# Kernel optimization log

Hardware: AMD Instinct MI355X
Metric: run time of the kernel (lower is better)

## Reference

```python
import jax, jax.numpy as jnp
import numpy as np

N_NODES = 50000
N_EDGES = 800000
HIDDEN = 256          # hidden_size == output_size (same `inputs` feeds all projections)
NUM_HEADS = 8
D_K = HIDDEN // NUM_HEADS  # 32
SCALE = float(np.sqrt(D_K))


def setup_inputs() -> dict:
    key = jax.random.key(0)
    ks = jax.random.split(key, 8)
    w_std = 1.0 / np.sqrt(HIDDEN)
    inputs = jax.random.normal(ks[0], (N_NODES, HIDDEN), jnp.float32)
    src = jax.random.randint(ks[1], (N_EDGES,), 0, N_NODES, dtype=jnp.int32)
    # guarantee every node has >= 1 in-edge (avoid 0/0 in normalization)
    dst_rand = jax.random.randint(ks[2], (N_EDGES - N_NODES,), 0, N_NODES, dtype=jnp.int32)
    dst = jnp.concatenate([jnp.arange(N_NODES, dtype=jnp.int32), dst_rand])
    Wq = jax.random.normal(ks[3], (HIDDEN, HIDDEN), jnp.float32) * w_std
    bq = jnp.zeros((HIDDEN,), jnp.float32)
    Wk = jax.random.normal(ks[4], (HIDDEN, HIDDEN), jnp.float32) * w_std
    Wv = jax.random.normal(ks[5], (HIDDEN, HIDDEN), jnp.float32) * w_std
    Wo = jax.random.normal(ks[6], (HIDDEN, HIDDEN), jnp.float32) * w_std
    bo = jnp.zeros((HIDDEN,), jnp.float32)
    return {"inputs": inputs, "Wq": Wq, "bq": bq, "Wk": Wk, "Wv": Wv,
            "Wo": Wo, "bo": bo, "src": src, "dst": dst}


def reference(inputs, Wq, bq, Wk, Wv, Wo, bo, src, dst):
    n = inputs.shape[0]
    # projections (dropout is identity in eval mode)
    q = (inputs @ Wq.T + bq).reshape(n, NUM_HEADS, D_K)
    k = (inputs @ Wk.T).reshape(n, NUM_HEADS, D_K)
    v = (inputs @ Wv.T).reshape(n, NUM_HEADS, D_K)
    # edge-wise dot product score: k[src] . q[dst]  -> [E, H]
    score = jnp.einsum('ehd,ehd->eh', k[src], q[dst])
    score = jnp.exp(jnp.clip(score / SCALE, -10.0, 10.0))
    # weighted segment-sum aggregation over in-edges of each dst node
    wv = jax.ops.segment_sum(v[src] * score[..., None], dst, num_segments=n)  # [N,H,dk]
    z = jax.ops.segment_sum(score, dst, num_segments=n)                        # [N,H]
    o = (wv / z[..., None]).reshape(n, HIDDEN)
    return o @ Wo.T + bo
```

## Files before the change

kernel.cpp:

```cpp
#include <hip/hip_runtime.h>
#include <hip/hip_bf16.h>
#include <math.h>

#define HIDDEN 256
#define INV_SCALE 0.17677669529663687f

typedef __attribute__((ext_vector_type(8))) short short8;
typedef __attribute__((ext_vector_type(4))) float f32x4;
typedef const __attribute__((address_space(1))) unsigned int* gas_ptr;
typedef __attribute__((address_space(3))) unsigned int* las_ptr;

static __device__ __forceinline__ unsigned short f2bf(float x) {
  unsigned u = __float_as_uint(x);
  unsigned r = (u + 0x7FFF + ((u >> 16) & 1)) >> 16;
  return (unsigned short)r;
}
static __device__ __forceinline__ float bf2f(unsigned short u) {
  return __uint_as_float((unsigned)u << 16);
}


__global__ __launch_bounds__(256) void conv_a_kernel(const float* __restrict__ in,
                                                     unsigned short* __restrict__ out,
                                                     int total4) {
  int stride = gridDim.x * blockDim.x;
  for (int i = blockIdx.x * blockDim.x + threadIdx.x; i < total4; i += stride) {
    float4 f = ((const float4*)in)[i];
    ushort4 u;
    u.x = f2bf(f.x); u.y = f2bf(f.y); u.z = f2bf(f.z); u.w = f2bf(f.w);
    ((ushort4*)out)[i] = u;
  }
}

__global__ __launch_bounds__(256) void conv_w_kernel(const float* __restrict__ Wq,
                                                     const float* __restrict__ Wk,
                                                     const float* __restrict__ Wv,
                                                     const float* __restrict__ Wo,
                                                     unsigned short* __restrict__ wqkv,
                                                     unsigned short* __restrict__ wob) {
  int i = blockIdx.x * 256 + threadIdx.x;
  int m = i >> 16;
  int j = i & 65535;
  const float* s = (m == 0) ? Wq : (m == 1) ? Wk : (m == 2) ? Wv : Wo;
  unsigned short b = f2bf(s[j]);
  if (m < 3) wqkv[m * 65536 + j] = b;
  else wob[j] = b;
}


__global__ __launch_bounds__(256) void hist_kernel(const int* __restrict__ dst,
                                                   int* __restrict__ deg, int E) {
  int e = blockIdx.x * blockDim.x + threadIdx.x;
  if (e < E) atomicAdd(&deg[dst[e]], 1);
}

__global__ __launch_bounds__(256) void scan1_kernel(const int* __restrict__ deg,
                                                    int* __restrict__ offs,
                                                    int* __restrict__ bsums, int N) {
  __shared__ int s[256];
  int tid = threadIdx.x;
  int base = blockIdx.x * 1024 + tid * 4;
  int v0 = (base + 0 < N) ? deg[base + 0] : 0;
  int v1 = (base + 1 < N) ? deg[base + 1] : 0;
  int v2 = (base + 2 < N) ? deg[base + 2] : 0;
  int v3 = (base + 3 < N) ? deg[base + 3] : 0;
  int tsum = v0 + v1 + v2 + v3;
  s[tid] = tsum;
  __syncthreads();
  for (int off = 1; off < 256; off <<= 1) {
    int t = (tid >= off) ? s[tid - off] : 0;
    __syncthreads();
    s[tid] += t;
    __syncthreads();
  }
  int excl = s[tid] - tsum;
  if (base + 0 < N) offs[base + 0] = excl;
  if (base + 1 < N) offs[base + 1] = excl + v0;
  if (base + 2 < N) offs[base + 2] = excl + v0 + v1;
  if (base + 3 < N) offs[base + 3] = excl + v0 + v1 + v2;
  if (tid == 255) bsums[blockIdx.x] = s[255];
}

__global__ void scan2_kernel(int* __restrict__ bsums, int nb) {
  if (blockIdx.x == 0 && threadIdx.x == 0) {
    int run = 0;
    for (int b = 0; b < nb; ++b) { int t = bsums[b]; bsums[b] = run; run += t; }
  }
}

__global__ __launch_bounds__(256) void scan3_kernel(int* __restrict__ offs,
                                                    int* __restrict__ cursor,
                                                    const int* __restrict__ bsums,
                                                    int N, int E) {
  int i = blockIdx.x * blockDim.x + threadIdx.x;
  if (i < N) {
    int v = offs[i] + bsums[i >> 10];
    offs[i] = v;
    cursor[i] = v;
  }
  if (i == 0) offs[N] = E;
}

__global__ __launch_bounds__(256) void scatter_kernel(const int* __restrict__ dst,
                                                      const int* __restrict__ src,
                                                      int* __restrict__ cursor,
                                                      int* __restrict__ esrc, int E) {
  int e = blockIdx.x * blockDim.x + threadIdx.x;
  if (e < E) {
    int n = dst[e];
    int pos = atomicAdd(&cursor[n], 1);
    esrc[pos] = src[e];
  }
}

#define GBM 128
#define GBN 128
#define GBK 32
#define NKSTEP (HIDDEN / GBK)

template <int MODE>
__global__ __launch_bounds__(256) void mfma_gemm_kernel(const unsigned short* __restrict__ A,
                                                        const unsigned short* __restrict__ B,
                                                        const float* __restrict__ bias,
                                                        float* __restrict__ Cf,
                                                        unsigned short* __restrict__ Cq,
                                                        unsigned short* __restrict__ Ck,
                                                        unsigned short* __restrict__ Cv,
                                                        int M) {
  __shared__ unsigned short As[2][GBM][GBK];
  __shared__ unsigned short Bs[2][GBN][GBK];
  int tid = threadIdx.x;
  int lane = tid & 63;
  int wid = tid >> 6;
  int wm = wid >> 1, wn = wid & 1;
  int brow = blockIdx.x * GBM;
  int bcol = blockIdx.y * GBN;

  int srow = wid * 32 + (lane >> 2);
  int skoff = (lane & 3) * 8;
  const unsigned short* gA0 = &A[(size_t)(brow + srow) * HIDDEN + skoff];
  const unsigned short* gB0 = &B[(size_t)(bcol + srow) * HIDDEN + skoff];
  char* ldsA0 = (char*)&As[0][0][0] + wid * 2048;
  char* ldsA1 = (char*)&As[1][0][0] + wid * 2048;
  char* ldsB0 = (char*)&Bs[0][0][0] + wid * 2048;
  char* ldsB1 = (char*)&Bs[1][0][0] + wid * 2048;

  f32x4 acc[4][4] = {};

  int fr = lane & 15;
  int kg = (lane >> 4) * 8;

  {
    const unsigned short* a = gA0;
    const unsigned short* b = gB0;
    __builtin_amdgcn_global_load_lds((gas_ptr)(const void*)a, (las_ptr)(void*)ldsA0, 16, 0, 0);
    __builtin_amdgcn_global_load_lds((gas_ptr)(const void*)(a + 16 * HIDDEN), (las_ptr)(void*)(ldsA0 + 1024), 16, 0, 0);
    __builtin_amdgcn_global_load_lds((gas_ptr)(const void*)b, (las_ptr)(void*)ldsB0, 16, 0, 0);
    __builtin_amdgcn_global_load_lds((gas_ptr)(const void*)(b + 16 * HIDDEN), (las_ptr)(void*)(ldsB0 + 1024), 16, 0, 0);
  }

#pragma unroll
  for (int t = 0; t < NKSTEP; ++t) {
    int p = t & 1;
    if (t + 1 < NKSTEP) {
      int k1 = (t + 1) * GBK;
      const unsigned short* a = gA0 + k1;
      const unsigned short* b = gB0 + k1;
      char* dA = p ? ldsA0 : ldsA1;
      char* dB = p ? ldsB0 : ldsB1;
      __builtin_amdgcn_global_load_lds((gas_ptr)(const void*)a, (las_ptr)(void*)dA, 16, 0, 0);
      __builtin_amdgcn_global_load_lds((gas_ptr)(const void*)(a + 16 * HIDDEN), (las_ptr)(void*)(dA + 1024), 16, 0, 0);
      __builtin_amdgcn_global_load_lds((gas_ptr)(const void*)b, (las_ptr)(void*)dB, 16, 0, 0);
      __builtin_amdgcn_global_load_lds((gas_ptr)(const void*)(b + 16 * HIDDEN), (las_ptr)(void*)(dB + 1024), 16, 0, 0);
      asm volatile("s_waitcnt vmcnt(4)" ::: "memory");
    } else {
      asm volatile("s_waitcnt vmcnt(0)" ::: "memory");
    }
    __builtin_amdgcn_s_barrier();
    __builtin_amdgcn_sched_barrier(0);
    short8 af[4], bfg[4];
#pragma unroll
    for (int mi = 0; mi < 4; ++mi)
      af[mi] = *(const short8*)&As[p][wm * 64 + mi * 16 + fr][kg];
#pragma unroll
    for (int ni = 0; ni < 4; ++ni)
      bfg[ni] = *(const short8*)&Bs[p][wn * 64 + ni * 16 + fr][kg];
#pragma unroll
    for (int mi = 0; mi < 4; ++mi)
#pragma unroll
      for (int ni = 0; ni < 4; ++ni)
        acc[mi][ni] = __builtin_amdgcn_mfma_f32_16x16x32_bf16(af[mi], bfg[ni], acc[mi][ni], 0, 0, 0);
    __builtin_amdgcn_s_barrier();
  }

  int fq = lane >> 4;
#pragma unroll
  for (int mi = 0; mi < 4; ++mi) {
#pragma unroll
    for (int ni = 0; ni < 4; ++ni) {
      int c = bcol + wn * 64 + ni * 16 + fr;
#pragma unroll
      for (int j = 0; j < 4; ++j) {
        int r = brow + wm * 64 + mi * 16 + fq * 4 + j;
        if (r < M) {
          float val = acc[mi][ni][j];
          if (MODE == 1) {
            Cf[(size_t)r * HIDDEN + c] = val + bias[c];
          } else {
            if (c < 256) Cq[(size_t)r * HIDDEN + c] = f2bf(val + bias[c]);
            else if (c < 512) Ck[(size_t)r * HIDDEN + (c - 256)] = f2bf(val);
            else Cv[(size_t)r * HIDDEN + (c - 512)] = f2bf(val);
          }
        }
      }
    }
  }
}

__global__ __launch_bounds__(256) void agg_kernel(const unsigned short* __restrict__ q,
                                                  const unsigned short* __restrict__ k,
                                                  const unsigned short* __restrict__ v,
                                                  const int* __restrict__ offs,
                                                  const int* __restrict__ esrc,
                                                  unsigned short* __restrict__ o, int N) {
  int n = blockIdx.x * 4 + (threadIdx.x >> 6);
  if (n >= N) return;
  int lane = threadIdx.x & 63;
  int half = lane >> 5;
  int l = lane & 31;

  float qf[8];
  {
    ushort4 qa = *(const ushort4*)&q[(size_t)n * HIDDEN + l * 8];
    ushort4 qb = *(const ushort4*)&q[(size_t)n * HIDDEN + l * 8 + 4];
    qf[0] = bf2f(qa.x); qf[1] = bf2f(qa.y); qf[2] = bf2f(qa.z); qf[3] = bf2f(qa.w);
    qf[4] = bf2f(qb.x); qf[5] = bf2f(qb.y); qf[6] = bf2f(qb.z); qf[7] = bf2f(qb.w);
  }

  int e0 = offs[n], e1 = offs[n + 1];
  float wv[8] = {};
  float z = 0.f;

  for (int idx = e0; idx < e1; idx += 2) {
    int my = idx + half;
    bool valid = my < e1;
    int s = esrc[valid ? my : idx];
    const ushort4* kp = (const ushort4*)&k[(size_t)s * HIDDEN + l * 8];
    const ushort4* vp = (const ushort4*)&v[(size_t)s * HIDDEN + l * 8];
    ushort4 ka = kp[0], kb = kp[1];
    ushort4 va = vp[0], vb = vp[1];
    float dot = qf[0] * bf2f(ka.x) + qf[1] * bf2f(ka.y) + qf[2] * bf2f(ka.z) + qf[3] * bf2f(ka.w)
              + qf[4] * bf2f(kb.x) + qf[5] * bf2f(kb.y) + qf[6] * bf2f(kb.z) + qf[7] * bf2f(kb.w);
    dot += __shfl_xor(dot, 1);
    dot += __shfl_xor(dot, 2);
    float e = 0.f;
    if (valid) e = __expf(fminf(fmaxf(dot * INV_SCALE, -10.f), 10.f));
    wv[0] += e * bf2f(va.x); wv[1] += e * bf2f(va.y);
    wv[2] += e * bf2f(va.z); wv[3] += e * bf2f(va.w);
    wv[4] += e * bf2f(vb.x); wv[5] += e * bf2f(vb.y);
    wv[6] += e * bf2f(vb.z); wv[7] += e * bf2f(vb.w);
    z += e;
  }

#pragma unroll
  for (int j = 0; j < 8; ++j) wv[j] += __shfl_xor(wv[j], 32);
  z += __shfl_xor(z, 32);

  if (half == 0) {
    float inv = 1.0f / z;
    ushort4 o0, o1;
    o0.x = f2bf(wv[0] * inv); o0.y = f2bf(wv[1] * inv);
    o0.z = f2bf(wv[2] * inv); o0.w = f2bf(wv[3] * inv);
    o1.x = f2bf(wv[4] * inv); o1.y = f2bf(wv[5] * inv);
    o1.z = f2bf(wv[6] * inv); o1.w = f2bf(wv[7] * inv);
    ushort4* op = (ushort4*)&o[(size_t)n * HIDDEN + l * 8];
    op[0] = o0; op[1] = o1;
  }
}


extern "C" void kernel_launch(void* const* d_in, const int* in_sizes, int n_in,
                              void* d_out, int out_size, void* d_ws, size_t ws_size,
                              hipStream_t stream) {
  const float* inputs = (const float*)d_in[0];
  const float* Wq = (const float*)d_in[1];
  const float* bq = (const float*)d_in[2];
  const float* Wk = (const float*)d_in[3];
  const float* Wv = (const float*)d_in[4];
  const float* Wo = (const float*)d_in[5];
  const float* bo = (const float*)d_in[6];
  const int* src = (const int*)d_in[7];
  const int* dst = (const int*)d_in[8];

  int N = in_sizes[0] / HIDDEN;
  int E = in_sizes[7];
  int Mpad = N + GBM;

  char* w = (char*)d_ws;
  unsigned short* a_bf = (unsigned short*)w; w += (size_t)Mpad * HIDDEN * 2;
  unsigned short* qb = (unsigned short*)w;   w += (size_t)N * HIDDEN * 2;
  unsigned short* kb = (unsigned short*)w;   w += (size_t)N * HIDDEN * 2;
  unsigned short* vb = (unsigned short*)w;   w += (size_t)N * HIDDEN * 2;
  unsigned short* ob = (unsigned short*)w;   w += (size_t)Mpad * HIDDEN * 2;
  unsigned short* wqkv = (unsigned short*)w; w += (size_t)768 * HIDDEN * 2;
  unsigned short* wob = (unsigned short*)w;  w += (size_t)256 * HIDDEN * 2;
  int* deg = (int*)w;    w += (size_t)N * 4;
  int* offs = (int*)w;   w += (size_t)(N + 4) * 4;
  int* cursor = (int*)w; w += (size_t)N * 4;
  int* esrc = (int*)w;   w += (size_t)E * 4;
  int* bsums = (int*)w;  w += 256 * 4;

  conv_a_kernel<<<2048, 256, 0, stream>>>(inputs, a_bf, N * (HIDDEN / 4));
  conv_w_kernel<<<1024, 256, 0, stream>>>(Wq, Wk, Wv, Wo, wqkv, wob);

  hipMemsetAsync(deg, 0, (size_t)N * 4, stream);
  int eb = (E + 255) / 256;
  hist_kernel<<<eb, 256, 0, stream>>>(dst, deg, E);
  int nb = (N + 1023) / 1024;
  scan1_kernel<<<nb, 256, 0, stream>>>(deg, offs, bsums, N);
  scan2_kernel<<<1, 64, 0, stream>>>(bsums, nb);
  scan3_kernel<<<(N + 255) / 256, 256, 0, stream>>>(offs, cursor, bsums, N, E);
  scatter_kernel<<<eb, 256, 0, stream>>>(dst, src, cursor, esrc, E);

  dim3 gqkv((N + GBM - 1) / GBM, 768 / GBN);
  mfma_gemm_kernel<0><<<gqkv, 256, 0, stream>>>(a_bf, wqkv, bq, nullptr, qb, kb, vb, N);

  agg_kernel<<<(N + 3) / 4, 256, 0, stream>>>(qb, kb, vb, offs, esrc, ob, N);

  dim3 gout((N + GBM - 1) / GBM, 256 / GBN);
  mfma_gemm_kernel<1><<<gout, 256, 0, stream>>>(ob, wob, bo, (float*)d_out, nullptr, nullptr, nullptr, N);
}
```

Measured before the change: 313.9 us.

## Widen GEMM N-tile to 256 and gather four edges per wave in aggregation

```diff
diff --git a/kernel.cpp b/kernel.cpp
--- a/kernel.cpp
+++ b/kernel.cpp
@@ -18,6 +18,8 @@
 static __device__ __forceinline__ float bf2f(unsigned short u) {
   return __uint_as_float((unsigned)u << 16);
 }
+
+#define GLL(gp, lp) __builtin_amdgcn_global_load_lds((gas_ptr)(const void*)(gp), (las_ptr)(void*)(lp), 16, 0, 0)
 
 
 __global__ __launch_bounds__(256) void conv_a_kernel(const float* __restrict__ in,
@@ -114,19 +116,19 @@
 }
 
 #define GBM 128
-#define GBN 128
+#define GBN 256
 #define GBK 32
 #define NKSTEP (HIDDEN / GBK)
 
 template <int MODE>
-__global__ __launch_bounds__(256) void mfma_gemm_kernel(const unsigned short* __restrict__ A,
-                                                        const unsigned short* __restrict__ B,
-                                                        const float* __restrict__ bias,
-                                                        float* __restrict__ Cf,
-                                                        unsigned short* __restrict__ Cq,
-                                                        unsigned short* __restrict__ Ck,
-                                                        unsigned short* __restrict__ Cv,
-                                                        int M) {
+__global__ __launch_bounds__(256, 2) void mfma_gemm_kernel(const unsigned short* __restrict__ A,
+                                                           const unsigned short* __restrict__ B,
+                                                           const float* __restrict__ bias,
+                                                           float* __restrict__ Cf,
+                                                           unsigned short* __restrict__ Cq,
+                                                           unsigned short* __restrict__ Ck,
+                                                           unsigned short* __restrict__ Cv,
+                                                           int M) {
   __shared__ unsigned short As[2][GBM][GBK];
   __shared__ unsigned short Bs[2][GBN][GBK];
   int tid = threadIdx.x;
@@ -136,59 +138,48 @@
   int brow = blockIdx.x * GBM;
   int bcol = blockIdx.y * GBN;
 
-  int srow = wid * 32 + (lane >> 2);
+  int srow = lane >> 2;
   int skoff = (lane & 3) * 8;
-  const unsigned short* gA0 = &A[(size_t)(brow + srow) * HIDDEN + skoff];
-  const unsigned short* gB0 = &B[(size_t)(bcol + srow) * HIDDEN + skoff];
-  char* ldsA0 = (char*)&As[0][0][0] + wid * 2048;
-  char* ldsA1 = (char*)&As[1][0][0] + wid * 2048;
-  char* ldsB0 = (char*)&Bs[0][0][0] + wid * 2048;
-  char* ldsB1 = (char*)&Bs[1][0][0] + wid * 2048;
-
-  f32x4 acc[4][4] = {};
-
+  const unsigned short* gA = &A[(size_t)(brow + wid * 32 + srow) * HIDDEN + skoff];
+  const unsigned short* gB = &B[(size_t)(bcol + wid * 64 + srow) * HIDDEN + skoff];
+  char* ldsA = (char*)&As[0][0][0] + wid * 2048;
+  char* ldsB = (char*)&Bs[0][0][0] + wid * 4096;
+
+  f32x4 acc[4][8] = {};
   int fr = lane & 15;
   int kg = (lane >> 4) * 8;
 
-  {
-    const unsigned short* a = gA0;
-    const unsigned short* b = gB0;
-    __builtin_amdgcn_global_load_lds((gas_ptr)(const void*)a, (las_ptr)(void*)ldsA0, 16, 0, 0);
-    __builtin_amdgcn_global_load_lds((gas_ptr)(const void*)(a + 16 * HIDDEN), (las_ptr)(void*)(ldsA0 + 1024), 16, 0, 0);
-    __builtin_amdgcn_global_load_lds((gas_ptr)(const void*)b, (las_ptr)(void*)ldsB0, 16, 0, 0);
-    __builtin_amdgcn_global_load_lds((gas_ptr)(const void*)(b + 16 * HIDDEN), (las_ptr)(void*)(ldsB0 + 1024), 16, 0, 0);
-  }
+  GLL(gA, ldsA); GLL(gA + 16 * HIDDEN, ldsA + 1024);
+  GLL(gB, ldsB); GLL(gB + 16 * HIDDEN, ldsB + 1024);
+  GLL(gB + 32 * HIDDEN, ldsB + 2048); GLL(gB + 48 * HIDDEN, ldsB + 3072);
 
 #pragma unroll
   for (int t = 0; t < NKSTEP; ++t) {
     int p = t & 1;
     if (t + 1 < NKSTEP) {
       int k1 = (t + 1) * GBK;
-      const unsigned short* a = gA0 + k1;
-      const unsigned short* b = gB0 + k1;
-      char* dA = p ? ldsA0 : ldsA1;
-      char* dB = p ? ldsB0 : ldsB1;
-      __builtin_amdgcn_global_load_lds((gas_ptr)(const void*)a, (las_ptr)(void*)dA, 16, 0, 0);
-      __builtin_amdgcn_global_load_lds((gas_ptr)(const void*)(a + 16 * HIDDEN), (las_ptr)(void*)(dA + 1024), 16, 0, 0);
-      __builtin_amdgcn_global_load_lds((gas_ptr)(const void*)b, (las_ptr)(void*)dB, 16, 0, 0);
-      __builtin_amdgcn_global_load_lds((gas_ptr)(const void*)(b + 16 * HIDDEN), (las_ptr)(void*)(dB + 1024), 16, 0, 0);
-      asm volatile("s_waitcnt vmcnt(4)" ::: "memory");
+      char* dA = ldsA + ((t + 1) & 1) * 8192;
+      char* dB = ldsB + ((t + 1) & 1) * 16384;
+      GLL(gA + k1, dA); GLL(gA + k1 + 16 * HIDDEN, dA + 1024);
+      GLL(gB + k1, dB); GLL(gB + k1 + 16 * HIDDEN, dB + 1024);
+      GLL(gB + k1 + 32 * HIDDEN, dB + 2048); GLL(gB + k1 + 48 * HIDDEN, dB + 3072);
+      asm volatile("s_waitcnt vmcnt(6)" ::: "memory");
     } else {
       asm volatile("s_waitcnt vmcnt(0)" ::: "memory");
     }
     __builtin_amdgcn_s_barrier();
     __builtin_amdgcn_sched_barrier(0);
-    short8 af[4], bfg[4];
+    short8 af[4], bfg[8];
 #pragma unroll
     for (int mi = 0; mi < 4; ++mi)
       af[mi] = *(const short8*)&As[p][wm * 64 + mi * 16 + fr][kg];
 #pragma unroll
-    for (int ni = 0; ni < 4; ++ni)
-      bfg[ni] = *(const short8*)&Bs[p][wn * 64 + ni * 16 + fr][kg];
+    for (int ni = 0; ni < 8; ++ni)
+      bfg[ni] = *(const short8*)&Bs[p][wn * 128 + ni * 16 + fr][kg];
 #pragma unroll
     for (int mi = 0; mi < 4; ++mi)
 #pragma unroll
-      for (int ni = 0; ni < 4; ++ni)
+      for (int ni = 0; ni < 8; ++ni)
         acc[mi][ni] = __builtin_amdgcn_mfma_f32_16x16x32_bf16(af[mi], bfg[ni], acc[mi][ni], 0, 0, 0);
     __builtin_amdgcn_s_barrier();
   }
@@ -197,8 +188,8 @@
 #pragma unroll
   for (int mi = 0; mi < 4; ++mi) {
 #pragma unroll
-    for (int ni = 0; ni < 4; ++ni) {
-      int c = bcol + wn * 64 + ni * 16 + fr;
+    for (int ni = 0; ni < 8; ++ni) {
+      int c = bcol + wn * 128 + ni * 16 + fr;
 #pragma unroll
       for (int j = 0; j < 4; ++j) {
         int r = brow + wm * 64 + mi * 16 + fq * 4 + j;
@@ -226,54 +217,66 @@
   int n = blockIdx.x * 4 + (threadIdx.x >> 6);
   if (n >= N) return;
   int lane = threadIdx.x & 63;
-  int half = lane >> 5;
-  int l = lane & 31;
-
-  float qf[8];
+  int qd = lane >> 4;
+  int l = lane & 15;
+
+  float qf[16];
   {
-    ushort4 qa = *(const ushort4*)&q[(size_t)n * HIDDEN + l * 8];
-    ushort4 qb = *(const ushort4*)&q[(size_t)n * HIDDEN + l * 8 + 4];
-    qf[0] = bf2f(qa.x); qf[1] = bf2f(qa.y); qf[2] = bf2f(qa.z); qf[3] = bf2f(qa.w);
-    qf[4] = bf2f(qb.x); qf[5] = bf2f(qb.y); qf[6] = bf2f(qb.z); qf[7] = bf2f(qb.w);
+    const short8* qp = (const short8*)&q[(size_t)n * HIDDEN + l * 16];
+    short8 q0 = qp[0], q1 = qp[1];
+#pragma unroll
+    for (int j = 0; j < 8; ++j) {
+      qf[j] = bf2f((unsigned short)q0[j]);
+      qf[8 + j] = bf2f((unsigned short)q1[j]);
+    }
   }
 
   int e0 = offs[n], e1 = offs[n + 1];
-  float wv[8] = {};
+  float wv[16] = {};
   float z = 0.f;
 
-  for (int idx = e0; idx < e1; idx += 2) {
-    int my = idx + half;
+  for (int idx = e0; idx < e1; idx += 4) {
+    int my = idx + qd;
     bool valid = my < e1;
-    int s = esrc[valid ? my : idx];
-    const ushort4* kp = (const ushort4*)&k[(size_t)s * HIDDEN + l * 8];
-    const ushort4* vp = (const ushort4*)&v[(size_t)s * HIDDEN + l * 8];
-    ushort4 ka = kp[0], kb = kp[1];
-    ushort4 va = vp[0], vb = vp[1];
-    float dot = qf[0] * bf2f(ka.x) + qf[1] * bf2f(ka.y) + qf[2] * bf2f(ka.z) + qf[3] * bf2f(ka.w)
-              + qf[4] * bf2f(kb.x) + qf[5] * bf2f(kb.y) + qf[6] * bf2f(kb.z) + qf[7] * bf2f(kb.w);
+    int s = esrc[valid ? my : (e1 - 1)];
+    const short8* kp = (const short8*)&k[(size_t)s * HIDDEN + l * 16];
+    const short8* vp = (const short8*)&v[(size_t)s * HIDDEN + l * 16];
+    short8 k0 = kp[0], k1 = kp[1];
+    short8 v0 = vp[0], v1 = vp[1];
+    float d0 = 0.f, d1 = 0.f;
+#pragma unroll
+    for (int j = 0; j < 8; ++j) {
+      d0 += qf[j] * bf2f((unsigned short)k0[j]);
+      d1 += qf[8 + j] * bf2f((unsigned short)k1[j]);
+    }
+    float dot = d0 + d1;
     dot += __shfl_xor(dot, 1);
-    dot += __shfl_xor(dot, 2);
-    float e = 0.f;
-    if (valid) e = __expf(fminf(fmaxf(dot * INV_SCALE, -10.f), 10.f));
-    wv[0] += e * bf2f(va.x); wv[1] += e * bf2f(va.y);
-    wv[2] += e * bf2f(va.z); wv[3] += e * bf2f(va.w);
-    wv[4] += e * bf2f(vb.x); wv[5] += e * bf2f(vb.y);
-    wv[6] += e * bf2f(vb.z); wv[7] += e * bf2f(vb.w);
+    float e = valid ? __expf(fminf(fmaxf(dot * INV_SCALE, -10.f), 10.f)) : 0.f;
+#pragma unroll
+    for (int j = 0; j < 8; ++j) {
+      wv[j] += e * bf2f((unsigned short)v0[j]);
+      wv[8 + j] += e * bf2f((unsigned short)v1[j]);
+    }
     z += e;
   }
 
 #pragma unroll
-  for (int j = 0; j < 8; ++j) wv[j] += __shfl_xor(wv[j], 32);
+  for (int j = 0; j < 16; ++j) {
+    wv[j] += __shfl_xor(wv[j], 16);
+    wv[j] += __shfl_xor(wv[j], 32);
+  }
+  z += __shfl_xor(z, 16);
   z += __shfl_xor(z, 32);
 
-  if (half == 0) {
+  if (qd == 0) {
     float inv = 1.0f / z;
-    ushort4 o0, o1;
-    o0.x = f2bf(wv[0] * inv); o0.y = f2bf(wv[1] * inv);
-    o0.z = f2bf(wv[2] * inv); o0.w = f2bf(wv[3] * inv);
-    o1.x = f2bf(wv[4] * inv); o1.y = f2bf(wv[5] * inv);
-    o1.z = f2bf(wv[6] * inv); o1.w = f2bf(wv[7] * inv);
-    ushort4* op = (ushort4*)&o[(size_t)n * HIDDEN + l * 8];
+    short8 o0, o1;
+#pragma unroll
+    for (int j = 0; j < 8; ++j) {
+      o0[j] = (short)f2bf(wv[j] * inv);
+      o1[j] = (short)f2bf(wv[8 + j] * inv);
+    }
+    short8* op = (short8*)&o[(size_t)n * HIDDEN + l * 16];
     op[0] = o0; op[1] = o1;
   }
 }
```

After: 319.2 us. No clear change (+1.7%).

## Keep A row-tile in registers and stream all B column tiles per block

Applied to the files above, without the earlier changes.

```diff
diff --git a/kernel.cpp b/kernel.cpp
--- a/kernel.cpp
+++ b/kernel.cpp
@@ -18,6 +18,8 @@
 static __device__ __forceinline__ float bf2f(unsigned short u) {
   return __uint_as_float((unsigned)u << 16);
 }
+
+#define GLL(gp, lp) __builtin_amdgcn_global_load_lds((gas_ptr)(const void*)(gp), (las_ptr)(void*)(lp), 16, 0, 0)
 
 
 __global__ __launch_bounds__(256) void conv_a_kernel(const float* __restrict__ in,
@@ -113,13 +115,8 @@
   }
 }
 
-#define GBM 128
-#define GBN 128
-#define GBK 32
-#define NKSTEP (HIDDEN / GBK)
-
 template <int MODE>
-__global__ __launch_bounds__(256) void mfma_gemm_kernel(const unsigned short* __restrict__ A,
+__global__ __launch_bounds__(256, 1) void gemm_apersist(const unsigned short* __restrict__ A,
                                                         const unsigned short* __restrict__ B,
                                                         const float* __restrict__ bias,
                                                         float* __restrict__ Cf,
@@ -127,93 +124,91 @@
                                                         unsigned short* __restrict__ Ck,
                                                         unsigned short* __restrict__ Cv,
                                                         int M) {
-  __shared__ unsigned short As[2][GBM][GBK];
-  __shared__ unsigned short Bs[2][GBN][GBK];
+  constexpr int NT = (MODE == 0) ? 6 : 2;
+  constexpr int NU = 2 * NT;
+  __shared__ unsigned short Bs[2][4][128][32];
   int tid = threadIdx.x;
   int lane = tid & 63;
   int wid = tid >> 6;
   int wm = wid >> 1, wn = wid & 1;
-  int brow = blockIdx.x * GBM;
-  int bcol = blockIdx.y * GBN;
-
-  int srow = wid * 32 + (lane >> 2);
-  int skoff = (lane & 3) * 8;
-  const unsigned short* gA0 = &A[(size_t)(brow + srow) * HIDDEN + skoff];
-  const unsigned short* gB0 = &B[(size_t)(bcol + srow) * HIDDEN + skoff];
-  char* ldsA0 = (char*)&As[0][0][0] + wid * 2048;
-  char* ldsA1 = (char*)&As[1][0][0] + wid * 2048;
-  char* ldsB0 = (char*)&Bs[0][0][0] + wid * 2048;
-  char* ldsB1 = (char*)&Bs[1][0][0] + wid * 2048;
-
-  f32x4 acc[4][4] = {};
-
+  int brow = blockIdx.x * 128;
   int fr = lane & 15;
   int kg = (lane >> 4) * 8;
 
-  {
-    const unsigned short* a = gA0;
-    const unsigned short* b = gB0;
-    __builtin_amdgcn_global_load_lds((gas_ptr)(const void*)a, (las_ptr)(void*)ldsA0, 16, 0, 0);
-    __builtin_amdgcn_global_load_lds((gas_ptr)(const void*)(a + 16 * HIDDEN), (las_ptr)(void*)(ldsA0 + 1024), 16, 0, 0);
-    __builtin_amdgcn_global_load_lds((gas_ptr)(const void*)b, (las_ptr)(void*)ldsB0, 16, 0, 0);
-    __builtin_amdgcn_global_load_lds((gas_ptr)(const void*)(b + 16 * HIDDEN), (las_ptr)(void*)(ldsB0 + 1024), 16, 0, 0);
-  }
-
-#pragma unroll
-  for (int t = 0; t < NKSTEP; ++t) {
-    int p = t & 1;
-    if (t + 1 < NKSTEP) {
-      int k1 = (t + 1) * GBK;
-      const unsigned short* a = gA0 + k1;
-      const unsigned short* b = gB0 + k1;
-      char* dA = p ? ldsA0 : ldsA1;
-      char* dB = p ? ldsB0 : ldsB1;
-      __builtin_amdgcn_global_load_lds((gas_ptr)(const void*)a, (las_ptr)(void*)dA, 16, 0, 0);
-      __builtin_amdgcn_global_load_lds((gas_ptr)(const void*)(a + 16 * HIDDEN), (las_ptr)(void*)(dA + 1024), 16, 0, 0);
-      __builtin_amdgcn_global_load_lds((gas_ptr)(const void*)b, (las_ptr)(void*)dB, 16, 0, 0);
-      __builtin_amdgcn_global_load_lds((gas_ptr)(const void*)(b + 16 * HIDDEN), (las_ptr)(void*)(dB + 1024), 16, 0, 0);
-      asm volatile("s_waitcnt vmcnt(4)" ::: "memory");
+  short8 af[8][4];
+#pragma unroll
+  for (int kk = 0; kk < 8; ++kk)
+#pragma unroll
+    for (int mi = 0; mi < 4; ++mi)
+      af[kk][mi] = *(const short8*)&A[(size_t)(brow + wm * 64 + mi * 16 + fr) * HIDDEN + kk * 32 + kg];
+
+  auto stageB = [&](int u) {
+    int ct = u >> 1, h = u & 1;
+    const unsigned short* gB = &B[(size_t)(ct * 128 + (lane >> 2)) * HIDDEN + (h * 4 + wid) * 32 + (lane & 3) * 8];
+    char* lb = (char*)&Bs[h][wid][0][0];
+#pragma unroll
+    for (int i = 0; i < 8; ++i)
+      GLL(gB + (size_t)(i * 16) * HIDDEN, lb + i * 1024);
+  };
+
+  f32x4 acc[4][4];
+#pragma unroll
+  for (int mi = 0; mi < 4; ++mi)
+#pragma unroll
+    for (int ni = 0; ni < 4; ++ni) acc[mi][ni] = (f32x4){0.f, 0.f, 0.f, 0.f};
+
+  stageB(0);
+
+#pragma unroll
+  for (int u = 0; u < NU; ++u) {
+    if (u + 1 < NU) {
+      stageB(u + 1);
+      asm volatile("s_waitcnt vmcnt(8)" ::: "memory");
     } else {
       asm volatile("s_waitcnt vmcnt(0)" ::: "memory");
     }
     __builtin_amdgcn_s_barrier();
     __builtin_amdgcn_sched_barrier(0);
-    short8 af[4], bfg[4];
-#pragma unroll
-    for (int mi = 0; mi < 4; ++mi)
-      af[mi] = *(const short8*)&As[p][wm * 64 + mi * 16 + fr][kg];
-#pragma unroll
-    for (int ni = 0; ni < 4; ++ni)
-      bfg[ni] = *(const short8*)&Bs[p][wn * 64 + ni * 16 + fr][kg];
-#pragma unroll
-    for (int mi = 0; mi < 4; ++mi)
+    int h = u & 1;
+#pragma unroll
+    for (int kkk = 0; kkk < 4; ++kkk) {
+      short8 bf4[4];
 #pragma unroll
       for (int ni = 0; ni < 4; ++ni)
-        acc[mi][ni] = __builtin_amdgcn_mfma_f32_16x16x32_bf16(af[mi], bfg[ni], acc[mi][ni], 0, 0, 0);
-    __builtin_amdgcn_s_barrier();
-  }
-
-  int fq = lane >> 4;
-#pragma unroll
-  for (int mi = 0; mi < 4; ++mi) {
-#pragma unroll
-    for (int ni = 0; ni < 4; ++ni) {
-      int c = bcol + wn * 64 + ni * 16 + fr;
-#pragma unroll
-      for (int j = 0; j < 4; ++j) {
-        int r = brow + wm * 64 + mi * 16 + fq * 4 + j;
-        if (r < M) {
-          float val = acc[mi][ni][j];
-          if (MODE == 1) {
-            Cf[(size_t)r * HIDDEN + c] = val + bias[c];
-          } else {
-            if (c < 256) Cq[(size_t)r * HIDDEN + c] = f2bf(val + bias[c]);
-            else if (c < 512) Ck[(size_t)r * HIDDEN + (c - 256)] = f2bf(val);
-            else Cv[(size_t)r * HIDDEN + (c - 512)] = f2bf(val);
+        bf4[ni] = *(const short8*)&Bs[h][kkk][wn * 64 + ni * 16 + fr][kg];
+#pragma unroll
+      for (int mi = 0; mi < 4; ++mi)
+#pragma unroll
+        for (int ni = 0; ni < 4; ++ni)
+          acc[mi][ni] = __builtin_amdgcn_mfma_f32_16x16x32_bf16(af[h * 4 + kkk][mi], bf4[ni], acc[mi][ni], 0, 0, 0);
+    }
+    if (u & 1) {
+      int ct = u >> 1;
+      int fq = lane >> 4;
+#pragma unroll
+      for (int mi = 0; mi < 4; ++mi) {
+#pragma unroll
+        for (int ni = 0; ni < 4; ++ni) {
+          int c = ct * 128 + wn * 64 + ni * 16 + fr;
+#pragma unroll
+          for (int j = 0; j < 4; ++j) {
+            int r = brow + wm * 64 + mi * 16 + fq * 4 + j;
+            if (r < M) {
+              float val = acc[mi][ni][j];
+              if (MODE == 1) {
+                Cf[(size_t)r * HIDDEN + c] = val + bias[c];
+              } else {
+                if (c < 256) Cq[(size_t)r * HIDDEN + c] = f2bf(val + bias[c]);
+                else if (c < 512) Ck[(size_t)r * HIDDEN + (c - 256)] = f2bf(val);
+                else Cv[(size_t)r * HIDDEN + (c - 512)] = f2bf(val);
+              }
+            }
           }
+          acc[mi][ni] = (f32x4){0.f, 0.f, 0.f, 0.f};
         }
       }
     }
+    __builtin_amdgcn_s_barrier();
   }
 }
 
@@ -294,7 +289,7 @@
 
   int N = in_sizes[0] / HIDDEN;
   int E = in_sizes[7];
-  int Mpad = N + GBM;
+  int Mpad = N + 128;
 
   char* w = (char*)d_ws;
   unsigned short* a_bf = (unsigned short*)w; w += (size_t)Mpad * HIDDEN * 2;
@@ -322,11 +317,10 @@
   scan3_kernel<<<(N + 255) / 256, 256, 0, stream>>>(offs, cursor, bsums, N, E);
   scatter_kernel<<<eb, 256, 0, stream>>>(dst, src, cursor, esrc, E);
 
-  dim3 gqkv((N + GBM - 1) / GBM, 768 / GBN);
-  mfma_gemm_kernel<0><<<gqkv, 256, 0, stream>>>(a_bf, wqkv, bq, nullptr, qb, kb, vb, N);
+  int gblocks = (N + 127) / 128;
+  gemm_apersist<0><<<gblocks, 256, 0, stream>>>(a_bf, wqkv, bq, nullptr, qb, kb, vb, N);
 
   agg_kernel<<<(N + 3) / 4, 256, 0, stream>>>(qb, kb, vb, offs, esrc, ob, N);
 
-  dim3 gout((N + GBM - 1) / GBM, 256 / GBN);
-  mfma_gemm_kernel<1><<<gout, 256, 0, stream>>>(ob, wob, bo, (float*)d_out, nullptr, nullptr, nullptr, N);
-}
+  gemm_apersist<1><<<gblocks, 256, 0, stream>>>(ob, wob, bo, (float*)d_out, nullptr, nullptr, nullptr, N);
+}
```

Measured after the change: 381.2 us. +21.5%, slower.
